# Optimization experiments

Hardware: AMD Instinct MI355X
Metric: run time of the kernel (lower is better)

The kernel has to match this reference:

```python
import jax, jax.numpy as jnp
import numpy as np


def setup_inputs() -> dict:
    key = jax.random.key(0)
    k1, k2, k3 = jax.random.split(key, 3)
    B, IN, EXP, K = 1024, 1024, 40, 7
    OUT = IN * EXP  # 40960
    x = jax.random.normal(k1, (B, IN), dtype=jnp.float32)
    # fixed fan-in projection matrix: K nonzeros per output row
    vals = jax.random.uniform(k2, (OUT, K), dtype=jnp.float32)
    idx = jax.random.randint(k3, (OUT, K), 0, IN, dtype=jnp.int32)
    return {"x": x, "vals": vals, "idx": idx}


def reference(x, vals, idx):
    # y[b, o] = sum_k vals[o, k] * x[b, idx[o, k]]
    # equivalent to (W_sparse @ x.T).T with W in COO, fixed fan-in K.
    # Loop over the small fixed fan-in K (=7) to avoid a [B, OUT, K] intermediate.
    K = idx.shape[1]
    y = x[:, idx[:, 0]] * vals[:, 0][None, :]  # [B, OUT]
    for k in range(1, K):
        y = y + x[:, idx[:, k]] * vals[:, k][None, :]
    return y
```

## Files before the change

kernel.cpp:

```cpp
#include <hip/hip_runtime.h>

#define BATCH   1024
#define IN      1024
#define OUT     40960
#define KF      7
#define BT      8
#define NO      4
#define THREADS 256
#define OTILE   (THREADS * NO)

__global__ __launch_bounds__(THREADS, 4)
void sparse_proj(const float* __restrict__ x, const float* __restrict__ vals,
                 const int* __restrict__ idx, float* __restrict__ y)
{
    __shared__ float xs[2 * IN * 4];

    const int t     = threadIdx.x;
    const int b0    = blockIdx.y * BT;
    const int obase = blockIdx.x * OTILE + t;

    {
        const int g  = t >> 7;
        const int i0 = t & 127;
        const float* xb = x + (size_t)(b0 + 4 * g) * IN;
        float* dstg = &xs[g * (IN * 4)];
#pragma unroll
        for (int j = 0; j < 8; ++j) {
            const int i = i0 + j * 128;
            float4 f;
            f.x = xb[0 * IN + i];
            f.y = xb[1 * IN + i];
            f.z = xb[2 * IN + i];
            f.w = xb[3 * IN + i];
            *(float4*)&dstg[i * 4] = f;
        }
    }
    __syncthreads();

    float acc[NO][BT];
#pragma unroll
    for (int no = 0; no < NO; ++no)
#pragma unroll
        for (int r = 0; r < BT; ++r) acc[no][r] = 0.0f;

#pragma unroll
    for (int no = 0; no < NO; ++no) {
        const int o = obase + no * THREADS;
        const int*   ip = idx  + (size_t)o * KF;
        const float* vp = vals + (size_t)o * KF;
#pragma unroll
        for (int k = 0; k < KF; ++k) {
            const int   i = ip[k];
            const float v = vp[k];
            const float4 a = *(const float4*)&xs[i * 4];
            const float4 b = *(const float4*)&xs[IN * 4 + i * 4];
            acc[no][0] = fmaf(v, a.x, acc[no][0]);
            acc[no][1] = fmaf(v, a.y, acc[no][1]);
            acc[no][2] = fmaf(v, a.z, acc[no][2]);
            acc[no][3] = fmaf(v, a.w, acc[no][3]);
            acc[no][4] = fmaf(v, b.x, acc[no][4]);
            acc[no][5] = fmaf(v, b.y, acc[no][5]);
            acc[no][6] = fmaf(v, b.z, acc[no][6]);
            acc[no][7] = fmaf(v, b.w, acc[no][7]);
        }
    }

#pragma unroll
    for (int r = 0; r < BT; ++r) {
        float* yr = y + (size_t)(b0 + r) * OUT;
#pragma unroll
        for (int no = 0; no < NO; ++no) {
            __builtin_nontemporal_store(acc[no][r], &yr[obase + no * THREADS]);
        }
    }
}

extern "C" void kernel_launch(void* const* d_in, const int* in_sizes, int n_in,
                              void* d_out, int out_size, void* d_ws, size_t ws_size,
                              hipStream_t stream) {
    const float* x    = (const float*)d_in[0];
    const float* vals = (const float*)d_in[1];
    const int*   idx  = (const int*)d_in[2];
    float*       y    = (float*)d_out;

    dim3 grid(OUT / OTILE, BATCH / BT);
    sparse_proj<<<grid, dim3(THREADS), 0, stream>>>(x, vals, idx, y);
}
```

Before: 194.7 us.

## Transpose x to batch-major and gather rows per output with wave-uniform indices

Adds a transpose kernel that writes x as [IN, BATCH] into workspace. The main kernel then maps each wave to 32 outputs and 64 batch lanes, loading a coalesced row of xT for each wave-uniform index (readfirstlane) instead of staging x in LDS per 8-batch tile. Results are staged through padded LDS so that y stores come out as 32-wide row segments. This removes the repeated per-block LDS fill of x but makes the gathers go through global memory/L2 and adds a second kernel launch.

```diff
diff --git a/kernel.cpp b/kernel.cpp
--- a/kernel.cpp
+++ b/kernel.cpp
@@ -4,74 +4,81 @@
 #define IN      1024
 #define OUT     40960
 #define KF      7
-#define BT      8
-#define NO      4
+#define OSTRIP  32
 #define THREADS 256
-#define OTILE   (THREADS * NO)
+#define LDS_STRIDE 36
+
+__global__ __launch_bounds__(256)
+void transpose_x(const float* __restrict__ x, float* __restrict__ xT)
+{
+    __shared__ float tile[64][65];
+    const int t  = threadIdx.x;
+    const int c  = t & 63;
+    const int r0 = t >> 6;
+    const int bx = blockIdx.x * 64;
+    const int by = blockIdx.y * 64;
+#pragma unroll
+    for (int rr = 0; rr < 16; ++rr) {
+        int r = r0 + rr * 4;
+        tile[r][c] = x[(size_t)(by + r) * IN + bx + c];
+    }
+    __syncthreads();
+#pragma unroll
+    for (int rr = 0; rr < 16; ++rr) {
+        int r = r0 + rr * 4;
+        xT[(size_t)(bx + r) * BATCH + by + c] = tile[c][r];
+    }
+}
 
 __global__ __launch_bounds__(THREADS, 4)
-void sparse_proj(const float* __restrict__ x, const float* __restrict__ vals,
-                 const int* __restrict__ idx, float* __restrict__ y)
+void sparse_proj_t(const float* __restrict__ xT, const float* __restrict__ vals,
+                   const int* __restrict__ idx, float* __restrict__ y)
 {
-    __shared__ float xs[2 * IN * 4];
+    __shared__ float tile[4 * 64 * LDS_STRIDE];
 
-    const int t     = threadIdx.x;
-    const int b0    = blockIdx.y * BT;
-    const int obase = blockIdx.x * OTILE + t;
+    const int lane  = threadIdx.x & 63;
+    const int w     = __builtin_amdgcn_readfirstlane(threadIdx.x >> 6);
+    const int btile = blockIdx.y * 64;
+    const int obase = blockIdx.x * (4 * OSTRIP) + w * OSTRIP;
+
+    const float* xTb   = xT + btile;
+    float*       wtile = &tile[w * 64 * LDS_STRIDE];
+
+    float4 acc4[OSTRIP / 4];
+
+#pragma unroll 2
+    for (int g = 0; g < OSTRIP / 4; ++g) {
+        float comp[4];
+#pragma unroll
+        for (int c = 0; c < 4; ++c) {
+            const int o = obase + g * 4 + c;
+            const int*   ip = idx  + (size_t)o * KF;
+            const float* vp = vals + (size_t)o * KF;
+            float a = 0.0f;
+#pragma unroll
+            for (int k = 0; k < KF; ++k) {
+                const int   si = __builtin_amdgcn_readfirstlane(ip[k]);
+                const float v  = vp[k];
+                a = fmaf(v, xTb[(size_t)si * BATCH + lane], a);
+            }
+            comp[c] = a;
+        }
+        acc4[g] = make_float4(comp[0], comp[1], comp[2], comp[3]);
+    }
 
     {
-        const int g  = t >> 7;
-        const int i0 = t & 127;
-        const float* xb = x + (size_t)(b0 + 4 * g) * IN;
-        float* dstg = &xs[g * (IN * 4)];
+        float4* myrow = (float4*)&wtile[lane * LDS_STRIDE];
 #pragma unroll
-        for (int j = 0; j < 8; ++j) {
-            const int i = i0 + j * 128;
-            float4 f;
-            f.x = xb[0 * IN + i];
-            f.y = xb[1 * IN + i];
-            f.z = xb[2 * IN + i];
-            f.w = xb[3 * IN + i];
-            *(float4*)&dstg[i * 4] = f;
-        }
+        for (int g = 0; g < OSTRIP / 4; ++g) myrow[g] = acc4[g];
     }
     __syncthreads();
 
-    float acc[NO][BT];
-#pragma unroll
-    for (int no = 0; no < NO; ++no)
-#pragma unroll
-        for (int r = 0; r < BT; ++r) acc[no][r] = 0.0f;
-
-#pragma unroll
-    for (int no = 0; no < NO; ++no) {
-        const int o = obase + no * THREADS;
-        const int*   ip = idx  + (size_t)o * KF;
-        const float* vp = vals + (size_t)o * KF;
-#pragma unroll
-        for (int k = 0; k < KF; ++k) {
-            const int   i = ip[k];
-            const float v = vp[k];
-            const float4 a = *(const float4*)&xs[i * 4];
-            const float4 b = *(const float4*)&xs[IN * 4 + i * 4];
-            acc[no][0] = fmaf(v, a.x, acc[no][0]);
-            acc[no][1] = fmaf(v, a.y, acc[no][1]);
-            acc[no][2] = fmaf(v, a.z, acc[no][2]);
-            acc[no][3] = fmaf(v, a.w, acc[no][3]);
-            acc[no][4] = fmaf(v, b.x, acc[no][4]);
-            acc[no][5] = fmaf(v, b.y, acc[no][5]);
-            acc[no][6] = fmaf(v, b.z, acc[no][6]);
-            acc[no][7] = fmaf(v, b.w, acc[no][7]);
-        }
-    }
-
-#pragma unroll
-    for (int r = 0; r < BT; ++r) {
-        float* yr = y + (size_t)(b0 + r) * OUT;
-#pragma unroll
-        for (int no = 0; no < NO; ++no) {
-            __builtin_nontemporal_store(acc[no][r], &yr[obase + no * THREADS]);
-        }
+#pragma unroll 4
+    for (int s = 0; s < 32; ++s) {
+        const int br = 2 * s + (lane >> 5);
+        const int oc = lane & 31;
+        const float val = wtile[br * LDS_STRIDE + oc];
+        __builtin_nontemporal_store(val, &y[(size_t)(btile + br) * OUT + obase + oc]);
     }
 }
 
@@ -82,7 +89,10 @@
     const float* vals = (const float*)d_in[1];
     const int*   idx  = (const int*)d_in[2];
     float*       y    = (float*)d_out;
+    float*       xT   = (float*)d_ws;
 
-    dim3 grid(OUT / OTILE, BATCH / BT);
-    sparse_proj<<<grid, dim3(THREADS), 0, stream>>>(x, vals, idx, y);
+    transpose_x<<<dim3(IN / 64, BATCH / 64), dim3(256), 0, stream>>>(x, xT);
+
+    dim3 grid(OUT / (4 * OSTRIP), BATCH / 64);
+    sparse_proj_t<<<grid, dim3(THREADS), 0, stream>>>(xT, vals, idx, y);
 }
```

Result: slower. 251.7 us (+29.3%).
